# Optimization experiments

Measured on AMD Instinct MI355X. Metric: run time of the kernel, lower is better.

Reference implementation:

```python
import jax, jax.numpy as jnp
import numpy as np

B, V, F_IN, F_HID = 1000000, 9, 5, 3


def setup_inputs() -> dict:
    key = jax.random.key(0)
    k1, k2, k3, k4, k5 = jax.random.split(key, 5)
    A = jax.random.uniform(k1, (B, V, V), dtype=jnp.float32)
    h0 = jax.random.uniform(k2, (B, V, F_IN), dtype=jnp.float32)
    # learned params (match torch init scales loosely)
    W = jax.random.uniform(k3, (F_IN, F_HID), dtype=jnp.float32) * 0.01
    fc_w = jax.random.normal(k4, (F_HID, 1), dtype=jnp.float32) * 0.1
    fc_b = jnp.zeros((1,), dtype=jnp.float32)
    return {"A": A, "h0": h0, "W": W, "fc_w": fc_w, "fc_b": fc_b}


def reference(A, h0, W, fc_w, fc_b):
    # GCN layer, batched (replaces per-sample Python loop)
    V_ = A.shape[-1]
    AI = A + jnp.eye(V_, dtype=A.dtype)                 # A + I, [B,V,V]
    deg = jnp.sum(AI, axis=-2)                          # torch.sum(AI, 0): column sums, [B,V]
    dinv = 1.0 / jnp.sqrt(deg)                          # diag of D^{-1/2}
    DAD = dinv[..., :, None] * AI * dinv[..., None, :]  # D^-1/2 (A+I) D^-1/2
    HW = jnp.einsum('bvf,fh->bvh', h0, W)               # H W
    h1 = jax.nn.relu(jnp.einsum('bvu,buh->bvh', DAD, HW))
    # graph pooling: sum over nodes
    h2 = jnp.sum(h1, axis=1)                            # [B, F_HID]
    return h2 @ fc_w + fc_b                             # [B, 1]
```

## Files before the change

kernel.cpp:

```cpp
#include <hip/hip_runtime.h>

#define NV 9
#define FIN 5
#define FHID 3
#define SPB 64
#define A_ELEMS (NV*NV)
#define H_ELEMS (NV*FIN)

__device__ __forceinline__ void load_lds16(const float* g, float* l) {
    __builtin_amdgcn_global_load_lds(
        (const __attribute__((address_space(1))) unsigned int*)g,
        (__attribute__((address_space(3))) unsigned int*)l, 16, 0, 0);
}

__global__ __launch_bounds__(64) void gcn_fused_kernel(
    const float* __restrict__ A, const float* __restrict__ h0,
    const float* __restrict__ W, const float* __restrict__ fc_w,
    const float* __restrict__ fc_b, float* __restrict__ out, int Btot)
{
    __shared__ float sA[SPB * A_ELEMS];
    __shared__ float sH[SPB * H_ELEMS];

    const int tid = threadIdx.x;
    const long long base = (long long)blockIdx.x * SPB;
    const int cnt = (Btot - (int)base < SPB) ? (Btot - (int)base) : SPB;

    const float* gA = A + base * A_ELEMS;
    const float* gH = h0 + base * H_ELEMS;

    if (cnt == SPB) {
#pragma unroll
        for (int j = 0; j < 20; j++)
            load_lds16(gA + j * 256 + tid * 4, sA + j * 256 + tid * 4);
        if (tid < 16)
            load_lds16(gA + 20 * 256 + tid * 4, sA + 20 * 256 + tid * 4);
#pragma unroll
        for (int j = 0; j < 11; j++)
            load_lds16(gH + j * 256 + tid * 4, sH + j * 256 + tid * 4);
        if (tid < 16)
            load_lds16(gH + 11 * 256 + tid * 4, sH + 11 * 256 + tid * 4);
    } else {
        const int nfltA = cnt * A_ELEMS;
        for (int i = tid; i < nfltA; i += SPB) sA[i] = gA[i];
        const int nfltH = cnt * H_ELEMS;
        for (int i = tid; i < nfltH; i += SPB) sH[i] = gH[i];
    }

    float Wr[FIN * FHID];
#pragma unroll
    for (int i = 0; i < FIN * FHID; i++) Wr[i] = W[i];
    const float fw0 = fc_w[0], fw1 = fc_w[1], fw2 = fc_w[2];
    const float fb = fc_b[0];

    asm volatile("s_waitcnt vmcnt(0)" ::: "memory");
    __syncthreads();

    if (tid >= cnt) return;

    const float* Ai = sA + tid * A_ELEMS;
    const float* Hi = sH + tid * H_ELEMS;

    float deg[NV];
#pragma unroll
    for (int j = 0; j < NV; j++) deg[j] = 1.0f;
#pragma unroll
    for (int i = 0; i < NV; i++) {
#pragma unroll
        for (int j = 0; j < NV; j++) deg[j] += Ai[i * NV + j];
    }
    float dinv[NV];
#pragma unroll
    for (int j = 0; j < NV; j++) dinv[j] = 1.0f / sqrtf(deg[j]);

    float G[NV * FHID];
#pragma unroll
    for (int u = 0; u < NV; u++) {
        float hr[FIN];
#pragma unroll
        for (int f = 0; f < FIN; f++) hr[f] = Hi[u * FIN + f];
#pragma unroll
        for (int h = 0; h < FHID; h++) {
            float acc = 0.0f;
#pragma unroll
            for (int f = 0; f < FIN; f++) acc += hr[f] * Wr[f * FHID + h];
            G[u * FHID + h] = dinv[u] * acc;
        }
    }

    float h2_0 = 0.0f, h2_1 = 0.0f, h2_2 = 0.0f;
#pragma unroll
    for (int v = 0; v < NV; v++) {
        float a0 = 0.0f, a1 = 0.0f, a2 = 0.0f;
#pragma unroll
        for (int u = 0; u < NV; u++) {
            float aiv = Ai[v * NV + u] + ((u == v) ? 1.0f : 0.0f);
            a0 += aiv * G[u * FHID + 0];
            a1 += aiv * G[u * FHID + 1];
            a2 += aiv * G[u * FHID + 2];
        }
        const float dv = dinv[v];
        a0 *= dv; a1 *= dv; a2 *= dv;
        h2_0 += fmaxf(a0, 0.0f);
        h2_1 += fmaxf(a1, 0.0f);
        h2_2 += fmaxf(a2, 0.0f);
    }

    out[base + tid] = h2_0 * fw0 + h2_1 * fw1 + h2_2 * fw2 + fb;
}

extern "C" void kernel_launch(void* const* d_in, const int* in_sizes, int n_in,
                              void* d_out, int out_size, void* d_ws, size_t ws_size,
                              hipStream_t stream) {
    const float* A    = (const float*)d_in[0];
    const float* h0   = (const float*)d_in[1];
    const float* W    = (const float*)d_in[2];
    const float* fc_w = (const float*)d_in[3];
    const float* fc_b = (const float*)d_in[4];
    float* out = (float*)d_out;

    const int Btot = in_sizes[0] / A_ELEMS;
    const int grid = (Btot + SPB - 1) / SPB;

    gcn_fused_kernel<<<grid, SPB, 0, stream>>>(A, h0, W, fc_w, fc_b, out, Btot);
}
```

Baseline: 530.1 us.

## Convert GCN kernel to persistent grid with double-buffered LDS prefetch

Turns the one-chunk-per-block kernel into a persistent kernel capped at 512 blocks. Each block walks chunks with a grid stride and prefetches the next chunk's A and h0 into a second LDS buffer while it computes on the current one. The adjacency tile is also copied into registers before use. This is meant to overlap global-to-LDS transfer with compute and to cut block launch overhead. In exchange, the doubled LDS footprint and the small grid leave only a couple of waves per CU, so fewer bytes may be in flight. The 81-element register array raises register pressure.

After: 550.1 us. +3.8%, slower.

```diff
diff --git a/kernel.cpp b/kernel.cpp
--- a/kernel.cpp
+++ b/kernel.cpp
@@ -6,6 +6,9 @@
 #define SPB 64
 #define A_ELEMS (NV*NV)
 #define H_ELEMS (NV*FIN)
+#define A_CHUNK (SPB*A_ELEMS)
+#define H_CHUNK (SPB*H_ELEMS)
+#define PERSIST_BLOCKS 512
 
 __device__ __forceinline__ void load_lds16(const float* g, float* l) {
     __builtin_amdgcn_global_load_lds(
@@ -13,38 +16,43 @@
         (__attribute__((address_space(3))) unsigned int*)l, 16, 0, 0);
 }
 
+__device__ __forceinline__ void stage_chunk(const float* __restrict__ gA,
+                                            const float* __restrict__ gH,
+                                            float* bA, float* bH,
+                                            int tid, int cnt)
+{
+    if (cnt == SPB) {
+#pragma unroll
+        for (int j = 0; j < 20; j++)
+            load_lds16(gA + j * 256 + tid * 4, bA + j * 256 + tid * 4);
+        if (tid < 16)
+            load_lds16(gA + 20 * 256 + tid * 4, bA + 20 * 256 + tid * 4);
+#pragma unroll
+        for (int j = 0; j < 11; j++)
+            load_lds16(gH + j * 256 + tid * 4, bH + j * 256 + tid * 4);
+        if (tid < 16)
+            load_lds16(gH + 11 * 256 + tid * 4, bH + 11 * 256 + tid * 4);
+    } else {
+        const int nA = cnt * A_ELEMS;
+        for (int i = tid; i < nA; i += SPB) bA[i] = gA[i];
+        const int nH = cnt * H_ELEMS;
+        for (int i = tid; i < nH; i += SPB) bH[i] = gH[i];
+    }
+}
+
 __global__ __launch_bounds__(64) void gcn_fused_kernel(
     const float* __restrict__ A, const float* __restrict__ h0,
     const float* __restrict__ W, const float* __restrict__ fc_w,
     const float* __restrict__ fc_b, float* __restrict__ out, int Btot)
 {
-    __shared__ float sA[SPB * A_ELEMS];
-    __shared__ float sH[SPB * H_ELEMS];
+    __shared__ float sA[2][A_CHUNK];
+    __shared__ float sH[2][H_CHUNK];
 
     const int tid = threadIdx.x;
-    const long long base = (long long)blockIdx.x * SPB;
-    const int cnt = (Btot - (int)base < SPB) ? (Btot - (int)base) : SPB;
-
-    const float* gA = A + base * A_ELEMS;
-    const float* gH = h0 + base * H_ELEMS;
-
-    if (cnt == SPB) {
-#pragma unroll
-        for (int j = 0; j < 20; j++)
-            load_lds16(gA + j * 256 + tid * 4, sA + j * 256 + tid * 4);
-        if (tid < 16)
-            load_lds16(gA + 20 * 256 + tid * 4, sA + 20 * 256 + tid * 4);
-#pragma unroll
-        for (int j = 0; j < 11; j++)
-            load_lds16(gH + j * 256 + tid * 4, sH + j * 256 + tid * 4);
-        if (tid < 16)
-            load_lds16(gH + 11 * 256 + tid * 4, sH + 11 * 256 + tid * 4);
-    } else {
-        const int nfltA = cnt * A_ELEMS;
-        for (int i = tid; i < nfltA; i += SPB) sA[i] = gA[i];
-        const int nfltH = cnt * H_ELEMS;
-        for (int i = tid; i < nfltH; i += SPB) sH[i] = gH[i];
-    }
+    const int nChunks = (Btot + SPB - 1) / SPB;
+    int c = blockIdx.x;
+    if (c >= nChunks) return;
+    const int stride = gridDim.x;
 
     float Wr[FIN * FHID];
 #pragma unroll
@@ -52,60 +60,85 @@
     const float fw0 = fc_w[0], fw1 = fc_w[1], fw2 = fc_w[2];
     const float fb = fc_b[0];
 
-    asm volatile("s_waitcnt vmcnt(0)" ::: "memory");
-    __syncthreads();
+    {
+        const long long base = (long long)c * SPB;
+        const int cnt = (Btot - (int)base < SPB) ? (Btot - (int)base) : SPB;
+        stage_chunk(A + base * A_ELEMS, h0 + base * H_ELEMS, sA[0], sH[0], tid, cnt);
+    }
+    int cur = 0;
 
-    if (tid >= cnt) return;
+    for (; c < nChunks; c += stride) {
+        asm volatile("s_waitcnt vmcnt(0)" ::: "memory");
+        __syncthreads();
 
-    const float* Ai = sA + tid * A_ELEMS;
-    const float* Hi = sH + tid * H_ELEMS;
+        const int cn = c + stride;
+        if (cn < nChunks) {
+            const long long nb = (long long)cn * SPB;
+            const int ncnt = (Btot - (int)nb < SPB) ? (Btot - (int)nb) : SPB;
+            stage_chunk(A + nb * A_ELEMS, h0 + nb * H_ELEMS,
+                        sA[cur ^ 1], sH[cur ^ 1], tid, ncnt);
+        }
 
-    float deg[NV];
+        const long long base = (long long)c * SPB;
+        const int cnt = (Btot - (int)base < SPB) ? (Btot - (int)base) : SPB;
+
+        if (tid < cnt) {
+            const float* Ai = sA[cur] + tid * A_ELEMS;
+            const float* Hi = sH[cur] + tid * H_ELEMS;
+
+            float a[A_ELEMS];
 #pragma unroll
-    for (int j = 0; j < NV; j++) deg[j] = 1.0f;
+            for (int i = 0; i < A_ELEMS; i++) a[i] = Ai[i];
+
+            float deg[NV];
 #pragma unroll
-    for (int i = 0; i < NV; i++) {
+            for (int j = 0; j < NV; j++) deg[j] = 1.0f;
 #pragma unroll
-        for (int j = 0; j < NV; j++) deg[j] += Ai[i * NV + j];
+            for (int i = 0; i < NV; i++) {
+#pragma unroll
+                for (int j = 0; j < NV; j++) deg[j] += a[i * NV + j];
+            }
+            float dinv[NV];
+#pragma unroll
+            for (int j = 0; j < NV; j++) dinv[j] = 1.0f / sqrtf(deg[j]);
+
+            float G[NV * FHID];
+#pragma unroll
+            for (int u = 0; u < NV; u++) {
+                float hr[FIN];
+#pragma unroll
+                for (int f = 0; f < FIN; f++) hr[f] = Hi[u * FIN + f];
+#pragma unroll
+                for (int h = 0; h < FHID; h++) {
+                    float acc = 0.0f;
+#pragma unroll
+                    for (int f = 0; f < FIN; f++) acc += hr[f] * Wr[f * FHID + h];
+                    G[u * FHID + h] = dinv[u] * acc;
+                }
+            }
+
+            float h2_0 = 0.0f, h2_1 = 0.0f, h2_2 = 0.0f;
+#pragma unroll
+            for (int v = 0; v < NV; v++) {
+                float a0 = 0.0f, a1 = 0.0f, a2 = 0.0f;
+#pragma unroll
+                for (int u = 0; u < NV; u++) {
+                    float aiv = a[v * NV + u] + ((u == v) ? 1.0f : 0.0f);
+                    a0 += aiv * G[u * FHID + 0];
+                    a1 += aiv * G[u * FHID + 1];
+                    a2 += aiv * G[u * FHID + 2];
+                }
+                const float dv = dinv[v];
+                a0 *= dv; a1 *= dv; a2 *= dv;
+                h2_0 += fmaxf(a0, 0.0f);
+                h2_1 += fmaxf(a1, 0.0f);
+                h2_2 += fmaxf(a2, 0.0f);
+            }
+
+            out[base + tid] = h2_0 * fw0 + h2_1 * fw1 + h2_2 * fw2 + fb;
+        }
+        cur ^= 1;
     }
-    float dinv[NV];
-#pragma unroll
-    for (int j = 0; j < NV; j++) dinv[j] = 1.0f / sqrtf(deg[j]);
-
-    float G[NV * FHID];
-#pragma unroll
-    for (int u = 0; u < NV; u++) {
-        float hr[FIN];
-#pragma unroll
-        for (int f = 0; f < FIN; f++) hr[f] = Hi[u * FIN + f];
-#pragma unroll
-        for (int h = 0; h < FHID; h++) {
-            float acc = 0.0f;
-#pragma unroll
-            for (int f = 0; f < FIN; f++) acc += hr[f] * Wr[f * FHID + h];
-            G[u * FHID + h] = dinv[u] * acc;
-        }
-    }
-
-    float h2_0 = 0.0f, h2_1 = 0.0f, h2_2 = 0.0f;
-#pragma unroll
-    for (int v = 0; v < NV; v++) {
-        float a0 = 0.0f, a1 = 0.0f, a2 = 0.0f;
-#pragma unroll
-        for (int u = 0; u < NV; u++) {
-            float aiv = Ai[v * NV + u] + ((u == v) ? 1.0f : 0.0f);
-            a0 += aiv * G[u * FHID + 0];
-            a1 += aiv * G[u * FHID + 1];
-            a2 += aiv * G[u * FHID + 2];
-        }
-        const float dv = dinv[v];
-        a0 *= dv; a1 *= dv; a2 *= dv;
-        h2_0 += fmaxf(a0, 0.0f);
-        h2_1 += fmaxf(a1, 0.0f);
-        h2_2 += fmaxf(a2, 0.0f);
-    }
-
-    out[base + tid] = h2_0 * fw0 + h2_1 * fw1 + h2_2 * fw2 + fb;
 }
 
 extern "C" void kernel_launch(void* const* d_in, const int* in_sizes, int n_in,
@@ -119,7 +152,8 @@
     float* out = (float*)d_out;
 
     const int Btot = in_sizes[0] / A_ELEMS;
-    const int grid = (Btot + SPB - 1) / SPB;
+    const int nChunks = (Btot + SPB - 1) / SPB;
+    const int grid = nChunks < PERSIST_BLOCKS ? nChunks : PERSIST_BLOCKS;
 
     gcn_fused_kernel<<<grid, SPB, 0, stream>>>(A, h0, W, fc_w, fc_b, out, Btot);
 }
```

## Replace LDS staging with direct per-thread vector global loads into registers

Applied to the files above, without the earlier changes.

Drops the shared-memory staging of A and h0 and the block-wide barrier. Each thread now loads its own sample's 81 adjacency values and 45 feature values straight into registers with 16-byte loads. Blocks grow from 64 to 256 threads. The aim is to lift the occupancy cap set by the 32KB of LDS per 64-thread block and to remove the barrier. The trade-off is that each wave's loads are strided and uncoalesced, so the kernel relies on the cache to combine them, and the larger per-thread register arrays raise register pressure.

Result: slower. 546.3 us (+3.1%).

```diff
diff --git a/kernel.cpp b/kernel.cpp
--- a/kernel.cpp
+++ b/kernel.cpp
@@ -3,88 +3,72 @@
 #define NV 9
 #define FIN 5
 #define FHID 3
-#define SPB 64
 #define A_ELEMS (NV*NV)
 #define H_ELEMS (NV*FIN)
+#define TPB 256
 
-__device__ __forceinline__ void load_lds16(const float* g, float* l) {
-    __builtin_amdgcn_global_load_lds(
-        (const __attribute__((address_space(1))) unsigned int*)g,
-        (__attribute__((address_space(3))) unsigned int*)l, 16, 0, 0);
+__device__ __forceinline__ float4 ld16(const float* p) {
+    float4 v;
+    __builtin_memcpy(&v, p, 16);
+    return v;
 }
 
-__global__ __launch_bounds__(64) void gcn_fused_kernel(
+__global__ __launch_bounds__(TPB, 2) void gcn_direct_kernel(
     const float* __restrict__ A, const float* __restrict__ h0,
     const float* __restrict__ W, const float* __restrict__ fc_w,
     const float* __restrict__ fc_b, float* __restrict__ out, int Btot)
 {
-    __shared__ float sA[SPB * A_ELEMS];
-    __shared__ float sH[SPB * H_ELEMS];
+    const int i = blockIdx.x * TPB + threadIdx.x;
+    if (i >= Btot) return;
 
-    const int tid = threadIdx.x;
-    const long long base = (long long)blockIdx.x * SPB;
-    const int cnt = (Btot - (int)base < SPB) ? (Btot - (int)base) : SPB;
+    const float* __restrict__ Ai = A  + (long long)i * A_ELEMS;
+    const float* __restrict__ Hi = h0 + (long long)i * H_ELEMS;
 
-    const float* gA = A + base * A_ELEMS;
-    const float* gH = h0 + base * H_ELEMS;
-
-    if (cnt == SPB) {
+    float a[A_ELEMS];
 #pragma unroll
-        for (int j = 0; j < 20; j++)
-            load_lds16(gA + j * 256 + tid * 4, sA + j * 256 + tid * 4);
-        if (tid < 16)
-            load_lds16(gA + 20 * 256 + tid * 4, sA + 20 * 256 + tid * 4);
-#pragma unroll
-        for (int j = 0; j < 11; j++)
-            load_lds16(gH + j * 256 + tid * 4, sH + j * 256 + tid * 4);
-        if (tid < 16)
-            load_lds16(gH + 11 * 256 + tid * 4, sH + 11 * 256 + tid * 4);
-    } else {
-        const int nfltA = cnt * A_ELEMS;
-        for (int i = tid; i < nfltA; i += SPB) sA[i] = gA[i];
-        const int nfltH = cnt * H_ELEMS;
-        for (int i = tid; i < nfltH; i += SPB) sH[i] = gH[i];
+    for (int j = 0; j < 20; j++) {
+        float4 v = ld16(Ai + 4 * j);
+        a[4*j+0] = v.x; a[4*j+1] = v.y; a[4*j+2] = v.z; a[4*j+3] = v.w;
     }
+    a[80] = Ai[80];
 
     float Wr[FIN * FHID];
 #pragma unroll
-    for (int i = 0; i < FIN * FHID; i++) Wr[i] = W[i];
+    for (int k = 0; k < FIN * FHID; k++) Wr[k] = W[k];
     const float fw0 = fc_w[0], fw1 = fc_w[1], fw2 = fc_w[2];
     const float fb = fc_b[0];
 
-    asm volatile("s_waitcnt vmcnt(0)" ::: "memory");
-    __syncthreads();
-
-    if (tid >= cnt) return;
-
-    const float* Ai = sA + tid * A_ELEMS;
-    const float* Hi = sH + tid * H_ELEMS;
+    float G[NV * FHID];
+#pragma unroll
+    for (int u = 0; u < NV; u++) {
+        float4 v = ld16(Hi + u * FIN);
+        const float h4 = Hi[u * FIN + 4];
+        const float hr[FIN] = {v.x, v.y, v.z, v.w, h4};
+#pragma unroll
+        for (int h = 0; h < FHID; h++) {
+            float acc = 0.0f;
+#pragma unroll
+            for (int f = 0; f < FIN; f++) acc += hr[f] * Wr[f * FHID + h];
+            G[u * FHID + h] = acc;
+        }
+    }
 
     float deg[NV];
 #pragma unroll
     for (int j = 0; j < NV; j++) deg[j] = 1.0f;
 #pragma unroll
-    for (int i = 0; i < NV; i++) {
+    for (int r = 0; r < NV; r++) {
 #pragma unroll
-        for (int j = 0; j < NV; j++) deg[j] += Ai[i * NV + j];
+        for (int j = 0; j < NV; j++) deg[j] += a[r * NV + j];
     }
     float dinv[NV];
 #pragma unroll
     for (int j = 0; j < NV; j++) dinv[j] = 1.0f / sqrtf(deg[j]);
 
-    float G[NV * FHID];
 #pragma unroll
     for (int u = 0; u < NV; u++) {
-        float hr[FIN];
 #pragma unroll
-        for (int f = 0; f < FIN; f++) hr[f] = Hi[u * FIN + f];
-#pragma unroll
-        for (int h = 0; h < FHID; h++) {
-            float acc = 0.0f;
-#pragma unroll
-            for (int f = 0; f < FIN; f++) acc += hr[f] * Wr[f * FHID + h];
-            G[u * FHID + h] = dinv[u] * acc;
-        }
+        for (int h = 0; h < FHID; h++) G[u * FHID + h] *= dinv[u];
     }
 
     float h2_0 = 0.0f, h2_1 = 0.0f, h2_2 = 0.0f;
@@ -93,19 +77,18 @@
         float a0 = 0.0f, a1 = 0.0f, a2 = 0.0f;
 #pragma unroll
         for (int u = 0; u < NV; u++) {
-            float aiv = Ai[v * NV + u] + ((u == v) ? 1.0f : 0.0f);
+            const float aiv = a[v * NV + u] + ((u == v) ? 1.0f : 0.0f);
             a0 += aiv * G[u * FHID + 0];
             a1 += aiv * G[u * FHID + 1];
             a2 += aiv * G[u * FHID + 2];
         }
         const float dv = dinv[v];
-        a0 *= dv; a1 *= dv; a2 *= dv;
-        h2_0 += fmaxf(a0, 0.0f);
-        h2_1 += fmaxf(a1, 0.0f);
-        h2_2 += fmaxf(a2, 0.0f);
+        h2_0 += fmaxf(a0 * dv, 0.0f);
+        h2_1 += fmaxf(a1 * dv, 0.0f);
+        h2_2 += fmaxf(a2 * dv, 0.0f);
     }
 
-    out[base + tid] = h2_0 * fw0 + h2_1 * fw1 + h2_2 * fw2 + fb;
+    out[i] = h2_0 * fw0 + h2_1 * fw1 + h2_2 * fw2 + fb;
 }
 
 extern "C" void kernel_launch(void* const* d_in, const int* in_sizes, int n_in,
@@ -119,7 +102,7 @@
     float* out = (float*)d_out;
 
     const int Btot = in_sizes[0] / A_ELEMS;
-    const int grid = (Btot + SPB - 1) / SPB;
+    const int grid = (Btot + TPB - 1) / TPB;
 
-    gcn_fused_kernel<<<grid, SPB, 0, stream>>>(A, h0, W, fc_w, fc_b, out, Btot);
+    gcn_direct_kernel<<<grid, TPB, 0, stream>>>(A, h0, W, fc_w, fc_b, out, Btot);
 }
```
